# Performance work log

Measured on AMD Instinct MI355X. Metric: run time of the kernel, lower is better.

The kernel has to match this reference:

```python
import jax, jax.numpy as jnp
import numpy as np

K = 16          # filter order (number of Laplacian powers)
MLP_OUT = 16    # mlp_hid == mlp_out for mlp_nlayers == 1
D_PE = 64       # phi output dim
BN_EPS = 1e-5
B, N, M = 8, 1024, 128
E = 131072


def setup_inputs() -> dict:
    key = jax.random.key(0)
    ks = jax.random.split(key, 12)
    # Symmetric, spectrally-bounded Laplacian surrogate so 15 matrix powers stay finite.
    A = jax.random.normal(ks[0], (B, N, N), dtype=jnp.float32)
    Lap = (A + jnp.swapaxes(A, -1, -2)) * (0.5 / jnp.sqrt(jnp.float32(N)))
    W = jax.random.normal(ks[1], (B, N, M), dtype=jnp.float32)
    edge_index = jax.random.randint(ks[2], (2, E), 0, B * N, dtype=jnp.int64)
    batch = jnp.repeat(jnp.arange(B, dtype=jnp.int64), N)
    # MLP layer (k -> MLP_OUT) + BatchNorm affine params
    lin_w = jax.random.normal(ks[3], (K, MLP_OUT), dtype=jnp.float32) / jnp.sqrt(jnp.float32(K))
    lin_b = jnp.zeros((MLP_OUT,), dtype=jnp.float32)
    bn_gamma = jnp.ones((MLP_OUT,), dtype=jnp.float32)
    bn_beta = jnp.zeros((MLP_OUT,), dtype=jnp.float32)
    # phi: GIN-style 2-layer MLP after neighbor aggregation
    phi_w1 = jax.random.normal(ks[4], (MLP_OUT, D_PE), dtype=jnp.float32) / jnp.sqrt(jnp.float32(MLP_OUT))
    phi_b1 = jnp.zeros((D_PE,), dtype=jnp.float32)
    phi_w2 = jax.random.normal(ks[5], (D_PE, D_PE), dtype=jnp.float32) / jnp.sqrt(jnp.float32(D_PE))
    phi_b2 = jnp.zeros((D_PE,), dtype=jnp.float32)
    return {"Lap": Lap, "W": W, "lin_w": lin_w, "lin_b": lin_b,
            "bn_gamma": bn_gamma, "bn_beta": bn_beta,
            "phi_w1": phi_w1, "phi_b1": phi_b1, "phi_w2": phi_w2, "phi_b2": phi_b2,
            "edge_index": edge_index, "batch": batch}


def _filter(S, W0):
    """Sequential power filter: returns [k, N, M] = [W0, S@W0, S^2@W0, ...]."""
    def step(out, _):
        nxt = S @ out
        return nxt, nxt
    _, rest = jax.lax.scan(step, W0, None, length=K - 1)
    return jnp.concatenate([W0[None], rest], axis=0)


def reference(Lap, W, lin_w, lin_b, bn_gamma, bn_beta,
              phi_w1, phi_b1, phi_w2, phi_b2, edge_index, batch):
    # Batched filter over all graphs: [B, k, N, M] -> [B, N, M, k]
    feat = jax.vmap(_filter)(Lap, W)
    feat = jnp.transpose(feat, (0, 2, 3, 1))
    # Linear over k -> MLP_OUT channels: [B, N, M, C]
    h = feat @ lin_w + lin_b
    # BatchNorm1d (training mode), per-graph statistics over (N, M) per channel,
    # matching the torch per-graph loop where BN sees [M, C, N].
    mean = jnp.mean(h, axis=(1, 2), keepdims=True)
    var = jnp.var(h, axis=(1, 2), keepdims=True)
    h = (h - mean) * jax.lax.rsqrt(var + BN_EPS) * bn_gamma + bn_beta
    h = jax.nn.relu(h)
    # phi: pool random-sample dim M, flatten graphs -> [N_sum, C]
    x = jnp.mean(h, axis=2).reshape(-1, h.shape[-1])
    src, dst = edge_index[0], edge_index[1]
    agg = jax.ops.segment_sum(x[src], dst, num_segments=x.shape[0])
    g = x + agg  # GIN aggregation
    out = jax.nn.relu(g @ phi_w1 + phi_b1) @ phi_w2 + phi_b2  # [N_sum, D_PE]
    return out
```

## Files before the change

kernel.cpp:

```cpp
#include <hip/hip_runtime.h>

#define B 8
#define N 1024
#define M 128
#define KF 16
#define C 16
#define DPE 64
#define NE 131072
#define NV (B*N)
#define NM (N*M)
#define BN_EPS 1e-5f

typedef short bf16x8 __attribute__((ext_vector_type(8)));
typedef float f32x4 __attribute__((ext_vector_type(4)));

__device__ inline unsigned short f2bf_rne(float f) {
    unsigned u = __float_as_uint(f);
    u += 0x7fffu + ((u >> 16) & 1u);
    return (unsigned short)(u >> 16);
}
__device__ inline float bf2f(unsigned short s) {
    return __uint_as_float((unsigned)s << 16);
}
__device__ inline void split_bf16(float v, unsigned short& hi, unsigned short& lo) {
    hi = f2bf_rne(v);
    float hf = __uint_as_float((unsigned)hi << 16);
    lo = f2bf_rne(v - hf);
}
union U4 { uint4 v; unsigned short s[8]; };
union U2 { uint2 v; unsigned short s[4]; };

__device__ __host__ inline size_t SF4(int b, int nsub, int ks, int hl, int l) {
    return ((((size_t)b * 64 + nsub) * 32 + ks) * 2 + hl) * 64 + l;
}
__device__ __host__ inline size_t PF4(int b, int msub, int ks, int hl, int l) {
    return ((((size_t)b * 8 + msub) * 32 + ks) * 2 + hl) * 64 + l;
}
#define PFBUF ((size_t)B * 8 * 32 * 2 * 64)

__global__ __launch_bounds__(256) void prep_all(const float* __restrict__ Lap,
                                                const float* __restrict__ W,
                                                const int* __restrict__ ei,
                                                uint4* __restrict__ Sf,
                                                uint4* __restrict__ Pf,
                                                unsigned short* __restrict__ feat,
                                                int* __restrict__ cnt) {
    __shared__ float T[32][33];
    int blk = blockIdx.x;
    int t = threadIdx.x;
    if (blk < 512) {
        int b = blk & 7, nb = blk >> 3;
        int nl = t >> 4, kg = t & 15;
        int n = nb * 16 + nl;
        const float* row = Lap + ((size_t)b * N + n) * N;
        #pragma unroll
        for (int jj = 0; jj < 8; jj++) {
            int koct = kg + 16 * jj;
            int k0 = koct * 8;
            float4 f0 = *(const float4*)(row + k0);
            float4 f1 = *(const float4*)(row + k0 + 4);
            float e[8] = {f0.x, f0.y, f0.z, f0.w, f1.x, f1.y, f1.z, f1.w};
            U4 hi, lo;
            #pragma unroll
            for (int j = 0; j < 8; j++) split_bf16(e[j], hi.s[j], lo.s[j]);
            int ks = k0 >> 5;
            int lf = nl + 16 * (koct & 3);
            Sf[SF4(b, nb, ks, 0, lf)] = hi.v;
            Sf[SF4(b, nb, ks, 1, lf)] = lo.v;
        }
    } else if (blk < 1536) {
        int r = blk - 512;
        int b = r & 7;
        int tile = r >> 3;
        int nt = tile & 31, mt = tile >> 5;
        int n0 = nt * 32, m0 = mt * 32;
        {
            int nl = t >> 3, mq = t & 7;
            float4 v = *(const float4*)(W + ((size_t)b * N + n0 + nl) * M + m0 + mq * 4);
            T[nl][mq * 4 + 0] = v.x; T[nl][mq * 4 + 1] = v.y;
            T[nl][mq * 4 + 2] = v.z; T[nl][mq * 4 + 3] = v.w;
        }
        __syncthreads();
        {
            int ml = t >> 3, nq = t & 7;
            U2 o;
            o.s[0] = f2bf_rne(T[nq * 4 + 0][ml]);
            o.s[1] = f2bf_rne(T[nq * 4 + 1][ml]);
            o.s[2] = f2bf_rne(T[nq * 4 + 2][ml]);
            o.s[3] = f2bf_rne(T[nq * 4 + 3][ml]);
            unsigned short* plane = feat + (size_t)b * KF * NM;
            *(uint2*)(plane + (size_t)(m0 + ml) * N + n0 + nq * 4) = o.v;
        }
    } else if (blk < 2048) {
        int r0 = blk - 1536;
        int b = r0 & 7;
        int r = (r0 >> 3) * 256 + t;
        int msub = r >> 11, ks = (r >> 6) & 31, l = r & 63;
        int m = 16 * msub + (l & 15);
        U4 hi, lo;
        #pragma unroll
        for (int j = 0; j < 8; j++) {
            int n = 32 * ks + 8 * (l >> 4) + j;
            float v = W[((size_t)b * N + n) * M + m];
            split_bf16(v, hi.s[j], lo.s[j]);
        }
        Pf[PF4(b, msub, ks, 0, l)] = hi.v;
        Pf[PF4(b, msub, ks, 1, l)] = lo.v;
    } else {
        int e = (blk - 2048) * 256 + t;
        bool is64 = (ei[1] == 0 && ei[3] == 0 && ei[5] == 0 && ei[7] == 0);
        int dst = is64 ? ei[2 * (NE + e)] : ei[NE + e];
        atomicAdd(&cnt[dst], 1);
    }
}

__global__ __launch_bounds__(512) void gemm_chain(const uint4* __restrict__ Sf,
                                                  uint4* __restrict__ PfA,
                                                  uint4* __restrict__ PfB,
                                                  unsigned short* __restrict__ feat,
                                                  unsigned* bar) {
    extern __shared__ __align__(16) char smem[];
    uint4* ldsS = (uint4*)smem;
    float* Dl = (float*)(smem + 131072);

    int b = blockIdx.x & 7, bx = blockIdx.x >> 3;
    int t = threadIdx.x;
    int w = t >> 6, lane = t & 63;
    int g = w >> 2, wq = w & 3;
    size_t sbase = SF4(b, 2 * bx, 0, 0, 0);
    int n0 = 32 * bx;

    #pragma unroll
    for (int i = 0; i < 16; i++) ldsS[t + 512 * i] = Sf[sbase + t + 512 * i];
    __syncthreads();

    #pragma unroll 1
    for (int k = 0; k < KF - 1; k++) {
        const uint4* PfIn = (k & 1) ? PfB : PfA;
        uint4* PfOut      = (k & 1) ? PfA : PfB;
        const uint4* Pw0 = PfIn + (size_t)(b * 8 + 2 * wq) * 4096 + (size_t)(16 * g) * 128;
        const uint4* Pw1 = Pw0 + 4096;

        f32x4 acc[2][2] = {};
        uint4 ph[2][2], pl[2][2];
        #pragma unroll
        for (int q = 0; q < 2; q++) {
            ph[q][0] = Pw0[(size_t)q * 128 + lane];
            pl[q][0] = Pw0[(size_t)q * 128 + 64 + lane];
            ph[q][1] = Pw1[(size_t)q * 128 + lane];
            pl[q][1] = Pw1[(size_t)q * 128 + 64 + lane];
        }
        #pragma unroll 2
        for (int ks = 0; ks < 16; ks++) {
            int kg = 16 * g + ks;
            uint4 a0h = ph[ks & 1][0], a0l = pl[ks & 1][0];
            uint4 a1h = ph[ks & 1][1], a1l = pl[ks & 1][1];
            if (ks < 14) {
                ph[ks & 1][0] = Pw0[(size_t)(ks + 2) * 128 + lane];
                pl[ks & 1][0] = Pw0[(size_t)(ks + 2) * 128 + 64 + lane];
                ph[ks & 1][1] = Pw1[(size_t)(ks + 2) * 128 + lane];
                pl[ks & 1][1] = Pw1[(size_t)(ks + 2) * 128 + 64 + lane];
            }
            bf16x8 b0h = __builtin_bit_cast(bf16x8, ldsS[kg * 128 + lane]);
            bf16x8 b0l = __builtin_bit_cast(bf16x8, ldsS[kg * 128 + 64 + lane]);
            bf16x8 b1h = __builtin_bit_cast(bf16x8, ldsS[4096 + kg * 128 + lane]);
            bf16x8 b1l = __builtin_bit_cast(bf16x8, ldsS[4096 + kg * 128 + 64 + lane]);
            bf16x8 A0h = __builtin_bit_cast(bf16x8, a0h);
            bf16x8 A0l = __builtin_bit_cast(bf16x8, a0l);
            bf16x8 A1h = __builtin_bit_cast(bf16x8, a1h);
            bf16x8 A1l = __builtin_bit_cast(bf16x8, a1l);
            acc[0][0] = __builtin_amdgcn_mfma_f32_16x16x32_bf16(A0h, b0h, acc[0][0], 0, 0, 0);
            acc[0][0] = __builtin_amdgcn_mfma_f32_16x16x32_bf16(A0h, b0l, acc[0][0], 0, 0, 0);
            acc[0][0] = __builtin_amdgcn_mfma_f32_16x16x32_bf16(A0l, b0h, acc[0][0], 0, 0, 0);
            acc[0][1] = __builtin_amdgcn_mfma_f32_16x16x32_bf16(A0h, b1h, acc[0][1], 0, 0, 0);
            acc[0][1] = __builtin_amdgcn_mfma_f32_16x16x32_bf16(A0h, b1l, acc[0][1], 0, 0, 0);
            acc[0][1] = __builtin_amdgcn_mfma_f32_16x16x32_bf16(A0l, b1h, acc[0][1], 0, 0, 0);
            acc[1][0] = __builtin_amdgcn_mfma_f32_16x16x32_bf16(A1h, b0h, acc[1][0], 0, 0, 0);
            acc[1][0] = __builtin_amdgcn_mfma_f32_16x16x32_bf16(A1h, b0l, acc[1][0], 0, 0, 0);
            acc[1][0] = __builtin_amdgcn_mfma_f32_16x16x32_bf16(A1l, b0h, acc[1][0], 0, 0, 0);
            acc[1][1] = __builtin_amdgcn_mfma_f32_16x16x32_bf16(A1h, b1h, acc[1][1], 0, 0, 0);
            acc[1][1] = __builtin_amdgcn_mfma_f32_16x16x32_bf16(A1h, b1l, acc[1][1], 0, 0, 0);
            acc[1][1] = __builtin_amdgcn_mfma_f32_16x16x32_bf16(A1l, b1h, acc[1][1], 0, 0, 0);
        }

        if (g == 1) {
            #pragma unroll
            for (int mi = 0; mi < 2; mi++)
                #pragma unroll
                for (int ni = 0; ni < 2; ni++)
                    #pragma unroll
                    for (int r = 0; r < 4; r++) {
                        int m = 32 * wq + 16 * mi + 4 * (lane >> 4) + r;
                        int c = 16 * ni + (lane & 15);
                        Dl[m * 36 + c] = acc[mi][ni][r];
                    }
        }
        __syncthreads();
        if (g == 0) {
            #pragma unroll
            for (int mi = 0; mi < 2; mi++)
                #pragma unroll
                for (int ni = 0; ni < 2; ni++)
                    #pragma unroll
                    for (int r = 0; r < 4; r++) {
                        int m = 32 * wq + 16 * mi + 4 * (lane >> 4) + r;
                        int c = 16 * ni + (lane & 15);
                        Dl[m * 36 + c] += acc[mi][ni][r];
                    }
        }
        __syncthreads();
        {
            int m = t >> 2, c0 = (t & 3) * 8;
            U4 o;
            #pragma unroll
            for (int j = 0; j < 8; j++) o.s[j] = f2bf_rne(Dl[m * 36 + c0 + j]);
            unsigned short* plane = feat + ((size_t)b * KF + (k + 1)) * NM + (size_t)m * N + n0 + c0;
            *(uint4*)plane = o.v;
        }
        if (k < KF - 2) {
            {
                int l = t & 63;
                int m = 16 * w + (l & 15);
                int ncol = 8 * (l >> 4);
                float4 v0 = *(const float4*)&Dl[m * 36 + ncol];
                float4 v1 = *(const float4*)&Dl[m * 36 + ncol + 4];
                float e[8] = {v0.x, v0.y, v0.z, v0.w, v1.x, v1.y, v1.z, v1.w};
                U4 hi, lo;
                #pragma unroll
                for (int j = 0; j < 8; j++) split_bf16(e[j], hi.s[j], lo.s[j]);
                PfOut[PF4(b, w, bx, 0, l)] = hi.v;
                PfOut[PF4(b, w, bx, 1, l)] = lo.v;
            }
            __syncthreads();
            if (t == 0) {
                __hip_atomic_fetch_add(&bar[b * 32], 1u, __ATOMIC_RELAXED,
                                       __HIP_MEMORY_SCOPE_AGENT);
                unsigned target = 32u * (unsigned)(k + 1);
                while (__hip_atomic_load(&bar[b * 32], __ATOMIC_RELAXED,
                                         __HIP_MEMORY_SCOPE_AGENT) < target)
                    __builtin_amdgcn_s_sleep(1);
            }
            __syncthreads();
            asm volatile("buffer_inv sc0\n\ts_waitcnt vmcnt(0)" ::: "memory");
        } else {
            __syncthreads();
        }
    }
}

__global__ __launch_bounds__(256) void bn_stats(const unsigned short* __restrict__ feat,
                                                const float* __restrict__ lin_w,
                                                const float* __restrict__ lin_b,
                                                float* __restrict__ stats) {
    __shared__ float wls[KF * C];
    __shared__ float red[4][2][C];
    int t = threadIdx.x;
    wls[t] = lin_w[t];
    __syncthreads();
    int b = blockIdx.x & 7;
    int i = (blockIdx.x >> 3) * 256 + t;
    const uint2* fb = (const uint2*)(feat + (size_t)b * KF * NM);

    float4 hacc[C];
    #pragma unroll
    for (int c = 0; c < C; c++) {
        float bb = lin_b[c];
        hacc[c] = make_float4(bb, bb, bb, bb);
    }
    for (int kk = 0; kk < KF; kk++) {
        U2 u; u.v = fb[(size_t)kk * (NM / 4) + i];
        float p0 = bf2f(u.s[0]), p1 = bf2f(u.s[1]), p2 = bf2f(u.s[2]), p3 = bf2f(u.s[3]);
        #pragma unroll
        for (int c = 0; c < C; c++) {
            float wv = wls[kk * C + c];
            hacc[c].x = fmaf(p0, wv, hacc[c].x);
            hacc[c].y = fmaf(p1, wv, hacc[c].y);
            hacc[c].z = fmaf(p2, wv, hacc[c].z);
            hacc[c].w = fmaf(p3, wv, hacc[c].w);
        }
    }
    float s[C], ss[C];
    #pragma unroll
    for (int c = 0; c < C; c++) {
        float4 h = hacc[c];
        s[c] = h.x + h.y + h.z + h.w;
        ss[c] = h.x * h.x + h.y * h.y + h.z * h.z + h.w * h.w;
    }
    #pragma unroll
    for (int off = 32; off > 0; off >>= 1)
        #pragma unroll
        for (int c = 0; c < C; c++) {
            s[c] += __shfl_down(s[c], off);
            ss[c] += __shfl_down(ss[c], off);
        }
    if ((t & 63) == 0) {
        int wv = t >> 6;
        #pragma unroll
        for (int c = 0; c < C; c++) { red[wv][0][c] = s[c]; red[wv][1][c] = ss[c]; }
    }
    __syncthreads();
    if (t < 32) {
        int which = t >> 4, c = t & 15;
        float v = red[0][which][c] + red[1][which][c] + red[2][which][c] + red[3][which][c];
        atomicAdd(&stats[b * 32 + which * 16 + c], v);
    }
}

__global__ __launch_bounds__(256) void bn_x(const unsigned short* __restrict__ feat,
                                            const float* __restrict__ lin_w,
                                            const float* __restrict__ lin_b,
                                            const float* __restrict__ gam,
                                            const float* __restrict__ bet,
                                            const float* __restrict__ stats,
                                            float* __restrict__ x) {
    __shared__ float wls[KF * C];
    __shared__ float red[8][32 * 17];
    int t = threadIdx.x;
    wls[t] = lin_w[t];
    __syncthreads();
    int grp = blockIdx.x;
    int b = grp & 7, n0 = (grp >> 3) * 32;
    int nl = t & 31, mg = t >> 5;
    int n = n0 + nl;

    const float inv_nm = 1.0f / (float)NM;
    float sc[C], sh[C], bb[C];
    #pragma unroll
    for (int c = 0; c < C; c++) {
        float mean = stats[b * 32 + c] * inv_nm;
        float var = stats[b * 32 + 16 + c] * inv_nm - mean * mean;
        sc[c] = gam[c] * rsqrtf(var + BN_EPS);
        sh[c] = bet[c] - mean * sc[c];
        bb[c] = lin_b[c];
    }
    const unsigned short* fb = feat + (size_t)b * KF * NM + n;
    float y[C] = {};
    for (int m = mg * 16; m < mg * 16 + 16; m++) {
        float p[KF];
        #pragma unroll
        for (int kk = 0; kk < KF; kk++) p[kk] = bf2f(fb[(size_t)kk * NM + (size_t)m * N]);
        #pragma unroll
        for (int c = 0; c < C; c++) {
            float h = bb[c];
            #pragma unroll
            for (int kk = 0; kk < KF; kk++) h = fmaf(p[kk], wls[kk * C + c], h);
            y[c] += fmaxf(fmaf(h, sc[c], sh[c]), 0.0f);
        }
    }
    #pragma unroll
    for (int c = 0; c < C; c++) red[mg][nl * 17 + c] = y[c];
    __syncthreads();
    #pragma unroll
    for (int q = 0; q < 2; q++) {
        int slot = t + q * 256;
        int snl = slot >> 4, c = slot & 15;
        float v = 0.0f;
        #pragma unroll
        for (int m8 = 0; m8 < 8; m8++) v += red[m8][snl * 17 + c];
        v *= (1.0f / (float)M);
        x[((size_t)b * N + n0 + snl) * C + c] = v;
    }
}

__global__ __launch_bounds__(256) void edge_scan(const int* __restrict__ cnt,
                                                 int* __restrict__ off, int* __restrict__ cur) {
    __shared__ int ss[256];
    int t = threadIdx.x;
    int base = t * 32;
    int local[32];
    int s = 0;
    #pragma unroll
    for (int i = 0; i < 32; i++) { local[i] = cnt[base + i]; s += local[i]; }
    ss[t] = s;
    __syncthreads();
    #pragma unroll
    for (int d = 1; d < 256; d <<= 1) {
        int v = (t >= d) ? ss[t - d] : 0;
        __syncthreads();
        ss[t] += v;
        __syncthreads();
    }
    int excl = ss[t] - s;
    #pragma unroll
    for (int i = 0; i < 32; i++) { off[base + i] = excl; cur[base + i] = excl; excl += local[i]; }
}

__global__ __launch_bounds__(256) void edge_fill(const int* __restrict__ ei,
                                                 int* __restrict__ cur, int* __restrict__ bucket) {
    int e = blockIdx.x * 256 + threadIdx.x;
    bool is64 = (ei[1] == 0 && ei[3] == 0 && ei[5] == 0 && ei[7] == 0);
    int src, dst;
    if (is64) { src = ei[2 * e]; dst = ei[2 * (NE + e)]; }
    else      { src = ei[e];     dst = ei[NE + e]; }
    int pos = atomicAdd(&cur[dst], 1);
    bucket[pos] = src;
}

__global__ __launch_bounds__(256) void phi_fused(const int* __restrict__ cnt,
                                                 const int* __restrict__ off,
                                                 const int* __restrict__ bucket,
                                                 const float* __restrict__ x,
                                                 const float* __restrict__ w1,
                                                 const float* __restrict__ b1,
                                                 const float* __restrict__ w2,
                                                 const float* __restrict__ b2,
                                                 float* __restrict__ out) {
    __shared__ float w1s[C * DPE];
    __shared__ float w2s[DPE * DPE];
    __shared__ float b2s[DPE];
    __shared__ float gsh[16][17];
    __shared__ float h1sh[16][DPE];
    int t = threadIdx.x;
    #pragma unroll
    for (int q = 0; q < 4; q++) w1s[t + q * 256] = w1[t + q * 256];
    #pragma unroll
    for (int q = 0; q < 16; q++) w2s[t + q * 256] = w2[t + q * 256];
    if (t < DPE) b2s[t] = b2[t];

    {
        int nl = t >> 4, c = t & 15;
        int n = blockIdx.x * 16 + nl;
        int o = off[n], d = cnt[n];
        float v = x[(size_t)n * C + c];
        int j = 0;
        for (; j + 4 <= d; j += 4) {
            int s0 = bucket[o + j], s1 = bucket[o + j + 1];
            int s2 = bucket[o + j + 2], s3 = bucket[o + j + 3];
            v += x[(size_t)s0 * C + c];
            v += x[(size_t)s1 * C + c];
            v += x[(size_t)s2 * C + c];
            v += x[(size_t)s3 * C + c];
        }
        for (; j < d; j++) v += x[(size_t)bucket[o + j] * C + c];
        gsh[nl][c] = v;
    }
    __syncthreads();
    #pragma unroll
    for (int q = 0; q < 4; q++) {
        int item = t + 256 * q;
        int node = item >> 6, j = item & 63;
        float h = b1[j];
        #pragma unroll
        for (int c = 0; c < C; c++) h = fmaf(gsh[node][c], w1s[c * DPE + j], h);
        h1sh[node][j] = fmaxf(h, 0.0f);
    }
    __syncthreads();
    #pragma unroll
    for (int q = 0; q < 4; q++) {
        int item = t + 256 * q;
        int node = item >> 6, d = item & 63;
        float o2 = b2s[d];
        #pragma unroll
        for (int j = 0; j < DPE; j++) o2 = fmaf(h1sh[node][j], w2s[j * DPE + d], o2);
        out[((size_t)blockIdx.x * 16 + node) * DPE + d] = o2;
    }
}

extern "C" void kernel_launch(void* const* d_in, const int* in_sizes, int n_in,
                              void* d_out, int out_size, void* d_ws, size_t ws_size,
                              hipStream_t stream) {
    const float* Lap   = (const float*)d_in[0];
    const float* W     = (const float*)d_in[1];
    const float* lin_w = (const float*)d_in[2];
    const float* lin_b = (const float*)d_in[3];
    const float* gam   = (const float*)d_in[4];
    const float* bet   = (const float*)d_in[5];
    const float* w1    = (const float*)d_in[6];
    const float* b1    = (const float*)d_in[7];
    const float* w2    = (const float*)d_in[8];
    const float* b2    = (const float*)d_in[9];
    const int*   ei    = (const int*)d_in[10];

    char* wsb = (char*)d_ws;
    unsigned short* feat = (unsigned short*)wsb;
    uint4* Sf    = (uint4*)(wsb + ((size_t)32 << 20));
    uint4* Pf    = (uint4*)(wsb + ((size_t)64 << 20));
    float* stats = (float*)(wsb + ((size_t)72 << 20));
    unsigned* bar = (unsigned*)(stats + 256);
    float* x     = stats + 2048;
    int*   cnt   = (int*)(x + (size_t)NV * C);
    int*   off   = cnt + NV;
    int*   cur   = off + NV;
    int*   bucket= cur + NV;
    float* out   = (float*)d_out;

    static bool attr_set = false;
    if (!attr_set) {
        hipFuncSetAttribute((const void*)gemm_chain,
                            hipFuncAttributeMaxDynamicSharedMemorySize, 149504);
        attr_set = true;
    }

    hipMemsetAsync(stats, 0, 8192, stream);
    hipMemsetAsync(cnt, 0, NV * sizeof(int), stream);
    prep_all<<<dim3(2560), 256, 0, stream>>>(Lap, W, ei, Sf, Pf, feat, cnt);
    gemm_chain<<<dim3(256), 512, 149504, stream>>>(Sf, Pf, Pf + PFBUF, feat, bar);
    bn_stats<<<dim3(1024), 256, 0, stream>>>(feat, lin_w, lin_b, stats);
    bn_x<<<dim3(256), 256, 0, stream>>>(feat, lin_w, lin_b, gam, bet, stats, x);
    edge_scan<<<dim3(1), 256, 0, stream>>>(cnt, off, cur);
    edge_fill<<<dim3(NE / 256), 256, 0, stream>>>(ei, cur, bucket);
    phi_fused<<<dim3(NV / 16), 256, 0, stream>>>(cnt, off, bucket, x, w1, b1, w2, b2, out);
}
```

Before: 293.3 us.

## Replace per-step grid barrier with per-block ready flags and fuse small kernels

The per-graph barrier between GEMM chain steps is replaced by per-block readiness counters. Each consumer waits only for the specific 32-row slice of P it is about to load, reading slices in a rotated order with a 4-deep prefetch. A read-done counter guards the double buffer against being overwritten before all readers finish. The edge scan is folded into the BN statistics kernel and the edge fill into the bn_x kernel, which cuts two launches and merges the memsets; the cost is more atomic polling and more complex cross-block ordering.

```diff
diff --git a/kernel.cpp b/kernel.cpp
--- a/kernel.cpp
+++ b/kernel.cpp
@@ -118,7 +118,8 @@
                                                   uint4* __restrict__ PfA,
                                                   uint4* __restrict__ PfB,
                                                   unsigned short* __restrict__ feat,
-                                                  unsigned* bar) {
+                                                  int* __restrict__ ready,
+                                                  int* __restrict__ rd) {
     extern __shared__ __align__(16) char smem[];
     uint4* ldsS = (uint4*)smem;
     float* Dl = (float*)(smem + 131072);
@@ -127,8 +128,10 @@
     int t = threadIdx.x;
     int w = t >> 6, lane = t & 63;
     int g = w >> 2, wq = w & 3;
+    int rot = bx & 15;
     size_t sbase = SF4(b, 2 * bx, 0, 0, 0);
     int n0 = 32 * bx;
+    int* rdy = ready + b * 32 + 16 * g;
 
     #pragma unroll
     for (int i = 0; i < 16; i++) ldsS[t + 512 * i] = Sf[sbase + t + 512 * i];
@@ -141,25 +144,57 @@
         const uint4* Pw0 = PfIn + (size_t)(b * 8 + 2 * wq) * 4096 + (size_t)(16 * g) * 128;
         const uint4* Pw1 = Pw0 + 4096;
 
+        asm volatile("buffer_inv sc0\n\ts_waitcnt vmcnt(0)" ::: "memory");
+
         f32x4 acc[2][2] = {};
-        uint4 ph[2][2], pl[2][2];
-        #pragma unroll
-        for (int q = 0; q < 2; q++) {
-            ph[q][0] = Pw0[(size_t)q * 128 + lane];
-            pl[q][0] = Pw0[(size_t)q * 128 + 64 + lane];
-            ph[q][1] = Pw1[(size_t)q * 128 + lane];
-            pl[q][1] = Pw1[(size_t)q * 128 + 64 + lane];
-        }
-        #pragma unroll 2
+        uint4 ph[4][2], pl[4][2];
+        int fl[4];
+        #pragma unroll
+        for (int q = 0; q < 4; q++)
+            fl[q] = (k > 0) ? __hip_atomic_load(rdy + ((q + rot) & 15),
+                                                __ATOMIC_RELAXED, __HIP_MEMORY_SCOPE_AGENT)
+                            : 0;
+        #pragma unroll
+        for (int q = 0; q < 4; q++) {
+            int ke = (q + rot) & 15;
+            if (k > 0) {
+                while (fl[q] < k) {
+                    __builtin_amdgcn_s_sleep(1);
+                    fl[q] = __hip_atomic_load(rdy + ke, __ATOMIC_RELAXED,
+                                              __HIP_MEMORY_SCOPE_AGENT);
+                }
+            }
+            ph[q][0] = Pw0[(size_t)ke * 128 + lane];
+            pl[q][0] = Pw0[(size_t)ke * 128 + 64 + lane];
+            ph[q][1] = Pw1[(size_t)ke * 128 + lane];
+            pl[q][1] = Pw1[(size_t)ke * 128 + 64 + lane];
+        }
+        int fnext = (k > 0) ? __hip_atomic_load(rdy + ((4 + rot) & 15),
+                                                __ATOMIC_RELAXED, __HIP_MEMORY_SCOPE_AGENT)
+                            : 0;
+
+        #pragma unroll 4
         for (int ks = 0; ks < 16; ks++) {
-            int kg = 16 * g + ks;
-            uint4 a0h = ph[ks & 1][0], a0l = pl[ks & 1][0];
-            uint4 a1h = ph[ks & 1][1], a1l = pl[ks & 1][1];
-            if (ks < 14) {
-                ph[ks & 1][0] = Pw0[(size_t)(ks + 2) * 128 + lane];
-                pl[ks & 1][0] = Pw0[(size_t)(ks + 2) * 128 + 64 + lane];
-                ph[ks & 1][1] = Pw1[(size_t)(ks + 2) * 128 + lane];
-                pl[ks & 1][1] = Pw1[(size_t)(ks + 2) * 128 + 64 + lane];
+            int slot = ks & 3;
+            int kg = 16 * g + ((ks + rot) & 15);
+            uint4 a0h = ph[slot][0], a0l = pl[slot][0];
+            uint4 a1h = ph[slot][1], a1l = pl[slot][1];
+            if (ks < 12) {
+                int kn = (ks + 4 + rot) & 15;
+                if (k > 0) {
+                    while (fnext < k) {
+                        __builtin_amdgcn_s_sleep(1);
+                        fnext = __hip_atomic_load(rdy + kn, __ATOMIC_RELAXED,
+                                                  __HIP_MEMORY_SCOPE_AGENT);
+                    }
+                }
+                ph[slot][0] = Pw0[(size_t)kn * 128 + lane];
+                pl[slot][0] = Pw0[(size_t)kn * 128 + 64 + lane];
+                ph[slot][1] = Pw1[(size_t)kn * 128 + lane];
+                pl[slot][1] = Pw1[(size_t)kn * 128 + 64 + lane];
+                if (ks < 11 && k > 0)
+                    fnext = __hip_atomic_load(rdy + ((ks + 5 + rot) & 15),
+                                              __ATOMIC_RELAXED, __HIP_MEMORY_SCOPE_AGENT);
             }
             bf16x8 b0h = __builtin_bit_cast(bf16x8, ldsS[kg * 128 + lane]);
             bf16x8 b0l = __builtin_bit_cast(bf16x8, ldsS[kg * 128 + 64 + lane]);
@@ -196,6 +231,9 @@
                     }
         }
         __syncthreads();
+        if (t == 0 && k < KF - 2)
+            __hip_atomic_fetch_add(rd + b * 16 + k, 1, __ATOMIC_RELAXED,
+                                   __HIP_MEMORY_SCOPE_AGENT);
         if (g == 0) {
             #pragma unroll
             for (int mi = 0; mi < 2; mi++)
@@ -208,6 +246,11 @@
                         Dl[m * 36 + c] += acc[mi][ni][r];
                     }
         }
+        if (t == 0 && k >= 1 && k < KF - 2) {
+            while (__hip_atomic_load(rd + b * 16 + k - 1, __ATOMIC_RELAXED,
+                                     __HIP_MEMORY_SCOPE_AGENT) < 32)
+                __builtin_amdgcn_s_sleep(1);
+        }
         __syncthreads();
         {
             int m = t >> 2, c0 = (t & 3) * 8;
@@ -218,47 +261,63 @@
             *(uint4*)plane = o.v;
         }
         if (k < KF - 2) {
-            {
-                int l = t & 63;
-                int m = 16 * w + (l & 15);
-                int ncol = 8 * (l >> 4);
-                float4 v0 = *(const float4*)&Dl[m * 36 + ncol];
-                float4 v1 = *(const float4*)&Dl[m * 36 + ncol + 4];
-                float e[8] = {v0.x, v0.y, v0.z, v0.w, v1.x, v1.y, v1.z, v1.w};
-                U4 hi, lo;
-                #pragma unroll
-                for (int j = 0; j < 8; j++) split_bf16(e[j], hi.s[j], lo.s[j]);
-                PfOut[PF4(b, w, bx, 0, l)] = hi.v;
-                PfOut[PF4(b, w, bx, 1, l)] = lo.v;
-            }
-            __syncthreads();
-            if (t == 0) {
-                __hip_atomic_fetch_add(&bar[b * 32], 1u, __ATOMIC_RELAXED,
-                                       __HIP_MEMORY_SCOPE_AGENT);
-                unsigned target = 32u * (unsigned)(k + 1);
-                while (__hip_atomic_load(&bar[b * 32], __ATOMIC_RELAXED,
-                                         __HIP_MEMORY_SCOPE_AGENT) < target)
-                    __builtin_amdgcn_s_sleep(1);
-            }
-            __syncthreads();
-            asm volatile("buffer_inv sc0\n\ts_waitcnt vmcnt(0)" ::: "memory");
-        } else {
-            __syncthreads();
-        }
-    }
-}
-
-__global__ __launch_bounds__(256) void bn_stats(const unsigned short* __restrict__ feat,
-                                                const float* __restrict__ lin_w,
-                                                const float* __restrict__ lin_b,
-                                                float* __restrict__ stats) {
+            int l = t & 63;
+            int m = 16 * w + (l & 15);
+            int ncol = 8 * (l >> 4);
+            float4 v0 = *(const float4*)&Dl[m * 36 + ncol];
+            float4 v1 = *(const float4*)&Dl[m * 36 + ncol + 4];
+            float e[8] = {v0.x, v0.y, v0.z, v0.w, v1.x, v1.y, v1.z, v1.w};
+            U4 hi, lo;
+            #pragma unroll
+            for (int j = 0; j < 8; j++) split_bf16(e[j], hi.s[j], lo.s[j]);
+            PfOut[PF4(b, w, bx, 0, l)] = hi.v;
+            PfOut[PF4(b, w, bx, 1, l)] = lo.v;
+        }
+        __syncthreads();
+        if (t == 0 && k < KF - 2)
+            __hip_atomic_store(ready + b * 32 + bx, k + 1, __ATOMIC_RELAXED,
+                               __HIP_MEMORY_SCOPE_AGENT);
+    }
+}
+
+__global__ __launch_bounds__(256) void bn_stats_scan(const unsigned short* __restrict__ feat,
+                                                     const float* __restrict__ lin_w,
+                                                     const float* __restrict__ lin_b,
+                                                     float* __restrict__ stats,
+                                                     const int* __restrict__ cnt,
+                                                     int* __restrict__ off,
+                                                     int* __restrict__ cur) {
     __shared__ float wls[KF * C];
     __shared__ float red[4][2][C];
+    __shared__ int ss[256];
     int t = threadIdx.x;
+    if (blockIdx.x < 8) {
+        if (blockIdx.x == 0) {
+            int base = t * 32;
+            int local[32];
+            int s = 0;
+            #pragma unroll
+            for (int i = 0; i < 32; i++) { local[i] = cnt[base + i]; s += local[i]; }
+            ss[t] = s;
+            __syncthreads();
+            #pragma unroll
+            for (int d = 1; d < 256; d <<= 1) {
+                int v = (t >= d) ? ss[t - d] : 0;
+                __syncthreads();
+                ss[t] += v;
+                __syncthreads();
+            }
+            int excl = ss[t] - s;
+            #pragma unroll
+            for (int i = 0; i < 32; i++) { off[base + i] = excl; cur[base + i] = excl; excl += local[i]; }
+        }
+        return;
+    }
+    int blk = blockIdx.x - 8;
     wls[t] = lin_w[t];
     __syncthreads();
-    int b = blockIdx.x & 7;
-    int i = (blockIdx.x >> 3) * 256 + t;
+    int b = blk & 7;
+    int i = (blk >> 3) * 256 + t;
     const uint2* fb = (const uint2*)(feat + (size_t)b * KF * NM);
 
     float4 hacc[C];
@@ -279,24 +338,24 @@
             hacc[c].w = fmaf(p3, wv, hacc[c].w);
         }
     }
-    float s[C], ss[C];
+    float s[C], ssq[C];
     #pragma unroll
     for (int c = 0; c < C; c++) {
         float4 h = hacc[c];
         s[c] = h.x + h.y + h.z + h.w;
-        ss[c] = h.x * h.x + h.y * h.y + h.z * h.z + h.w * h.w;
-    }
-    #pragma unroll
-    for (int off = 32; off > 0; off >>= 1)
+        ssq[c] = h.x * h.x + h.y * h.y + h.z * h.z + h.w * h.w;
+    }
+    #pragma unroll
+    for (int o = 32; o > 0; o >>= 1)
         #pragma unroll
         for (int c = 0; c < C; c++) {
-            s[c] += __shfl_down(s[c], off);
-            ss[c] += __shfl_down(ss[c], off);
+            s[c] += __shfl_down(s[c], o);
+            ssq[c] += __shfl_down(ssq[c], o);
         }
     if ((t & 63) == 0) {
         int wv = t >> 6;
         #pragma unroll
-        for (int c = 0; c < C; c++) { red[wv][0][c] = s[c]; red[wv][1][c] = ss[c]; }
+        for (int c = 0; c < C; c++) { red[wv][0][c] = s[c]; red[wv][1][c] = ssq[c]; }
     }
     __syncthreads();
     if (t < 32) {
@@ -306,16 +365,29 @@
     }
 }
 
-__global__ __launch_bounds__(256) void bn_x(const unsigned short* __restrict__ feat,
-                                            const float* __restrict__ lin_w,
-                                            const float* __restrict__ lin_b,
-                                            const float* __restrict__ gam,
-                                            const float* __restrict__ bet,
-                                            const float* __restrict__ stats,
-                                            float* __restrict__ x) {
+__global__ __launch_bounds__(256) void bnx_fill(const unsigned short* __restrict__ feat,
+                                                const float* __restrict__ lin_w,
+                                                const float* __restrict__ lin_b,
+                                                const float* __restrict__ gam,
+                                                const float* __restrict__ bet,
+                                                const float* __restrict__ stats,
+                                                float* __restrict__ x,
+                                                const int* __restrict__ ei,
+                                                int* __restrict__ cur,
+                                                int* __restrict__ bucket) {
     __shared__ float wls[KF * C];
     __shared__ float red[8][32 * 17];
     int t = threadIdx.x;
+    if (blockIdx.x >= 256) {
+        int e = (blockIdx.x - 256) * 256 + t;
+        bool is64 = (ei[1] == 0 && ei[3] == 0 && ei[5] == 0 && ei[7] == 0);
+        int src, dst;
+        if (is64) { src = ei[2 * e]; dst = ei[2 * (NE + e)]; }
+        else      { src = ei[e];     dst = ei[NE + e]; }
+        int pos = atomicAdd(&cur[dst], 1);
+        bucket[pos] = src;
+        return;
+    }
     wls[t] = lin_w[t];
     __syncthreads();
     int grp = blockIdx.x;
@@ -360,40 +432,6 @@
         v *= (1.0f / (float)M);
         x[((size_t)b * N + n0 + snl) * C + c] = v;
     }
-}
-
-__global__ __launch_bounds__(256) void edge_scan(const int* __restrict__ cnt,
-                                                 int* __restrict__ off, int* __restrict__ cur) {
-    __shared__ int ss[256];
-    int t = threadIdx.x;
-    int base = t * 32;
-    int local[32];
-    int s = 0;
-    #pragma unroll
-    for (int i = 0; i < 32; i++) { local[i] = cnt[base + i]; s += local[i]; }
-    ss[t] = s;
-    __syncthreads();
-    #pragma unroll
-    for (int d = 1; d < 256; d <<= 1) {
-        int v = (t >= d) ? ss[t - d] : 0;
-        __syncthreads();
-        ss[t] += v;
-        __syncthreads();
-    }
-    int excl = ss[t] - s;
-    #pragma unroll
-    for (int i = 0; i < 32; i++) { off[base + i] = excl; cur[base + i] = excl; excl += local[i]; }
-}
-
-__global__ __launch_bounds__(256) void edge_fill(const int* __restrict__ ei,
-                                                 int* __restrict__ cur, int* __restrict__ bucket) {
-    int e = blockIdx.x * 256 + threadIdx.x;
-    bool is64 = (ei[1] == 0 && ei[3] == 0 && ei[5] == 0 && ei[7] == 0);
-    int src, dst;
-    if (is64) { src = ei[2 * e]; dst = ei[2 * (NE + e)]; }
-    else      { src = ei[e];     dst = ei[NE + e]; }
-    int pos = atomicAdd(&cur[dst], 1);
-    bucket[pos] = src;
 }
 
 __global__ __launch_bounds__(256) void phi_fused(const int* __restrict__ cnt,
@@ -475,13 +513,15 @@
     unsigned short* feat = (unsigned short*)wsb;
     uint4* Sf    = (uint4*)(wsb + ((size_t)32 << 20));
     uint4* Pf    = (uint4*)(wsb + ((size_t)64 << 20));
-    float* stats = (float*)(wsb + ((size_t)72 << 20));
-    unsigned* bar = (unsigned*)(stats + 256);
-    float* x     = stats + 2048;
-    int*   cnt   = (int*)(x + (size_t)NV * C);
-    int*   off   = cnt + NV;
-    int*   cur   = off + NV;
-    int*   bucket= cur + NV;
+    char* tail   = wsb + ((size_t)72 << 20);
+    float* stats = (float*)tail;
+    int* ready   = (int*)(tail + 1024);
+    int* rd      = (int*)(tail + 2048);
+    int* cnt     = (int*)(tail + 8192);
+    float* x     = (float*)(tail + 40960);
+    int* off     = (int*)(x + (size_t)NV * C);
+    int* cur     = off + NV;
+    int* bucket  = cur + NV;
     float* out   = (float*)d_out;
 
     static bool attr_set = false;
@@ -491,13 +531,10 @@
         attr_set = true;
     }
 
-    hipMemsetAsync(stats, 0, 8192, stream);
-    hipMemsetAsync(cnt, 0, NV * sizeof(int), stream);
+    hipMemsetAsync(tail, 0, 40960, stream);
     prep_all<<<dim3(2560), 256, 0, stream>>>(Lap, W, ei, Sf, Pf, feat, cnt);
-    gemm_chain<<<dim3(256), 512, 149504, stream>>>(Sf, Pf, Pf + PFBUF, feat, bar);
-    bn_stats<<<dim3(1024), 256, 0, stream>>>(feat, lin_w, lin_b, stats);
-    bn_x<<<dim3(256), 256, 0, stream>>>(feat, lin_w, lin_b, gam, bet, stats, x);
-    edge_scan<<<dim3(1), 256, 0, stream>>>(cnt, off, cur);
-    edge_fill<<<dim3(NE / 256), 256, 0, stream>>>(ei, cur, bucket);
+    gemm_chain<<<dim3(256), 512, 149504, stream>>>(Sf, Pf, Pf + PFBUF, feat, ready, rd);
+    bn_stats_scan<<<dim3(1032), 256, 0, stream>>>(feat, lin_w, lin_b, stats, cnt, off, cur);
+    bnx_fill<<<dim3(768), 256, 0, stream>>>(feat, lin_w, lin_b, gam, bet, stats, x, ei, cur, bucket);
     phi_fused<<<dim3(NV / 16), 256, 0, stream>>>(cnt, off, bucket, x, w1, b1, w2, b2, out);
 }
```

Result: slower. 373.5 us (+27.4%).
